# Kernel optimization log

Measured on AMD Instinct MI355X. Metric: run time of the kernel, lower is better.

Reference implementation:

```python
import jax, jax.numpy as jnp
import numpy as np

HIDDEN = 2048
NUM_HEADS = 32
NUM_KV_HEADS = 8
HEAD_DIM = 64
HEADS_PER_KV = NUM_HEADS // NUM_KV_HEADS


def setup_inputs() -> dict:
    key = jax.random.key(0)
    ks = jax.random.split(key, 5)
    B, S = 2, 2048
    sd = 1.0 / np.sqrt(HIDDEN)
    x = jax.random.normal(ks[0], (B, S, HIDDEN), dtype=jnp.float32)
    wq = jax.random.normal(ks[1], (HIDDEN, NUM_HEADS * HEAD_DIM), dtype=jnp.float32) * sd
    wk = jax.random.normal(ks[2], (HIDDEN, NUM_KV_HEADS * HEAD_DIM), dtype=jnp.float32) * sd
    wv = jax.random.normal(ks[3], (HIDDEN, NUM_KV_HEADS * HEAD_DIM), dtype=jnp.float32) * sd
    wo = jax.random.normal(ks[4], (NUM_HEADS * HEAD_DIM, HIDDEN), dtype=jnp.float32) * sd
    return {"x": x, "wq": wq, "wk": wk, "wv": wv, "wo": wo}


def reference(x, wq, wk, wv, wo):
    B, S, _ = x.shape
    scale = 1.0 / np.sqrt(HEAD_DIM)
    # projections; self-attention (is_cross=False) so kv source = x
    q = (x @ wq).reshape(B, S, NUM_HEADS, HEAD_DIM)          # [B,S,H,D]
    k = (x @ wk).reshape(B, S, NUM_KV_HEADS, HEAD_DIM)        # [B,S,Hkv,D]
    v = (x @ wv).reshape(B, S, NUM_KV_HEADS, HEAD_DIM)
    # GQA: group query heads per kv head instead of repeating K/V
    q = q.reshape(B, S, NUM_KV_HEADS, HEADS_PER_KV, HEAD_DIM)
    # scores: [B, Hkv, G, Sq, Skv]
    scores = jnp.einsum('bqhgd,bkhd->bhgqk', q, k) * scale
    probs = jax.nn.softmax(scores, axis=-1)
    out = jnp.einsum('bhgqk,bkhd->bqhgd', probs, v)
    out = out.reshape(B, S, NUM_HEADS * HEAD_DIM)
    return out @ wo
```

## Files before the change

kernel.cpp:

```cpp
#include <hip/hip_runtime.h>
#include <hip/hip_bf16.h>


#define S_LEN 2048

typedef __hip_bfloat16 bf16;
using bf16x8 = __attribute__((ext_vector_type(8))) __bf16;
using f32x4  = __attribute__((ext_vector_type(4))) float;

__device__ inline unsigned short bf16_bits(float f) {
    union { __hip_bfloat16 h; unsigned short u; } cv;
    cv.h = __float2bfloat16(f);
    return cv.u;
}

__device__ inline float bits_to_f(unsigned short u) {
    union { __hip_bfloat16 h; unsigned short u; } cv;
    cv.u = u;
    return __bfloat162float(cv.h);
}

__device__ inline unsigned int cvt_pk_bf16(float lo, float hi) {
    unsigned int r;
    asm volatile("v_cvt_pk_bf16_f32 %0, %1, %2" : "=v"(r) : "v"(lo), "v"(hi));
    return r;
}

__device__ inline bf16x8 load_cvt8(const float* __restrict__ p) {
    f32x4 a = *(const f32x4*)p;
    f32x4 b = *(const f32x4*)(p + 4);
    union { bf16x8 v; unsigned short u[8]; } r;
    r.u[0] = bf16_bits(a[0]); r.u[1] = bf16_bits(a[1]);
    r.u[2] = bf16_bits(a[2]); r.u[3] = bf16_bits(a[3]);
    r.u[4] = bf16_bits(b[0]); r.u[5] = bf16_bits(b[1]);
    r.u[6] = bf16_bits(b[2]); r.u[7] = bf16_bits(b[3]);
    return r.v;
}

__device__ inline void gload_lds16(const bf16* g, bf16* l) {
    __builtin_amdgcn_global_load_lds((const __attribute__((address_space(1))) void*)g,
                                     (__attribute__((address_space(3))) void*)l,
                                     16, 0, 0);
}

__global__ __launch_bounds__(256) void prep_k(const float* __restrict__ x,
                                              const float* __restrict__ wq,
                                              const float* __restrict__ wk,
                                              const float* __restrict__ wv,
                                              bf16* __restrict__ xb,
                                              bf16* __restrict__ wqT,
                                              bf16* __restrict__ wkT,
                                              bf16* __restrict__ wvT) {
    __shared__ float tile[32][33];
    int bid = blockIdx.x;
    if (bid < 4096) {
        int i = bid * 256 + threadIdx.x;
        *(bf16x8*)(xb + (size_t)i * 8) = load_cvt8(x + (size_t)i * 8);
        return;
    }
    const float* in; bf16* out; int R, C, local;
    if (bid < 8192)      { local = bid - 4096; in = wq; out = wqT; R = 2048; C = 2048; }
    else if (bid < 9216) { local = bid - 8192; in = wk; out = wkT; R = 2048; C = 512;  }
    else                 { local = bid - 9216; in = wv; out = wvT; R = 2048; C = 512;  }
    int gx = C >> 5;
    int c0 = (local % gx) * 32, r0 = (local / gx) * 32;
    int tx = threadIdx.x & 31, ty = threadIdx.x >> 5;
#pragma unroll
    for (int p = 0; p < 4; ++p)
        tile[ty + p * 8][tx] = in[(size_t)(r0 + ty + p * 8) * C + c0 + tx];
    __syncthreads();
#pragma unroll
    for (int p = 0; p < 4; ++p)
        out[(size_t)(c0 + ty + p * 8) * R + r0 + tx] = __float2bfloat16(tile[tx][ty + p * 8]);
}

__global__ __launch_bounds__(256) void transpose_k(const float* __restrict__ in,
                                                   bf16* __restrict__ out,
                                                   int R, int C) {
    __shared__ float tile[32][33];
    int tx = threadIdx.x & 31, ty = threadIdx.x >> 5;
    int r0 = blockIdx.y * 32, c0 = blockIdx.x * 32;
#pragma unroll
    for (int p = 0; p < 4; ++p)
        tile[ty + p * 8][tx] = in[(size_t)(r0 + ty + p * 8) * C + c0 + tx];
    __syncthreads();
#pragma unroll
    for (int p = 0; p < 4; ++p)
        out[(size_t)(c0 + ty + p * 8) * R + r0 + tx] = __float2bfloat16(tile[tx][ty + p * 8]);
}

__global__ __launch_bounds__(256) void gemm_k(const bf16* __restrict__ A,
                                              const bf16* __restrict__ Bt,
                                              void* __restrict__ Cv,
                                              void* __restrict__ Cv2,
                                              void* __restrict__ Cv3,
                                              int M, int N, int K, int mode) {
    __shared__ bf16 As[128 * 32];
    __shared__ bf16 Bs[128 * 32];
    int tid  = threadIdx.x;
    int lane = tid & 63, wave = tid >> 6;
    int quad = lane >> 4, r = lane & 15;
    int wm = (wave >> 1) * 64, wn = (wave & 1) * 64;

    int nwg  = gridDim.x * gridDim.y;
    int flat = blockIdx.y * gridDim.x + blockIdx.x;
    int cpx  = nwg >> 3;
    int swz  = (flat & 7) * cpx + (flat >> 3);
    int m0 = (swz / gridDim.x) * 128, n0 = (swz % gridDim.x) * 128;

    f32x4 acc[4][4];
#pragma unroll
    for (int i = 0; i < 4; ++i)
#pragma unroll
        for (int j = 0; j < 4; ++j) acc[i][j] = (f32x4)0.0f;

    int rg = lane >> 2;
    int ck = (lane & 3) << 3;

    for (int k0 = 0; k0 < K; k0 += 32) {
#pragma unroll
        for (int g = 0; g < 2; ++g) {
            int grp = wave * 2 + g;
            int row = grp * 16 + rg;
            gload_lds16(A  + (size_t)(m0 + row) * K + k0 + ck, &As[grp * 512]);
            gload_lds16(Bt + (size_t)(n0 + row) * K + k0 + ck, &Bs[grp * 512]);
        }
        __syncthreads();
        bf16x8 af[4], bfr[4];
#pragma unroll
        for (int mt = 0; mt < 4; ++mt) af[mt]  = *(const bf16x8*)&As[(wm + mt * 16 + r) * 32 + quad * 8];
#pragma unroll
        for (int nt = 0; nt < 4; ++nt) bfr[nt] = *(const bf16x8*)&Bs[(wn + nt * 16 + r) * 32 + quad * 8];
#pragma unroll
        for (int mt = 0; mt < 4; ++mt)
#pragma unroll
            for (int nt = 0; nt < 4; ++nt)
                acc[mt][nt] = __builtin_amdgcn_mfma_f32_16x16x32_bf16(af[mt], bfr[nt], acc[mt][nt], 0, 0, 0);
        __syncthreads();
    }

    if (mode == 2) {
        float* C = (float*)Cv;
#pragma unroll
        for (int mt = 0; mt < 4; ++mt)
#pragma unroll
            for (int nt = 0; nt < 4; ++nt) {
                int row = m0 + wm + mt * 16 + quad * 4;
                int col = n0 + wn + nt * 16 + r;
#pragma unroll
                for (int i = 0; i < 4; ++i)
                    C[(size_t)(row + i) * N + col] = acc[mt][nt][i];
            }
    } else {
        if (n0 < 2048) {
            bf16* C = (bf16*)Cv;
#pragma unroll
            for (int mt = 0; mt < 4; ++mt)
#pragma unroll
                for (int nt = 0; nt < 4; ++nt) {
                    int row = m0 + wm + mt * 16 + quad * 4;
                    int col = n0 + wn + nt * 16 + r;
#pragma unroll
                    for (int i = 0; i < 4; ++i)
                        C[(size_t)(row + i) * 2048 + col] = __float2bfloat16(acc[mt][nt][i]);
                }
        } else if (n0 < 2560) {
            bf16* C = (bf16*)Cv2;
#pragma unroll
            for (int mt = 0; mt < 4; ++mt)
#pragma unroll
                for (int nt = 0; nt < 4; ++nt) {
                    int row = m0 + wm + mt * 16 + quad * 4;
                    int col = n0 - 2048 + wn + nt * 16 + r;
#pragma unroll
                    for (int i = 0; i < 4; ++i)
                        C[(size_t)(row + i) * 512 + col] = __float2bfloat16(acc[mt][nt][i]);
                }
        } else {
            unsigned short* C = (unsigned short*)Cv3;
#pragma unroll
            for (int mt = 0; mt < 4; ++mt)
#pragma unroll
                for (int nt = 0; nt < 4; ++nt) {
                    int rowb = m0 + wm + mt * 16 + quad * 4;
                    int col  = n0 - 2560 + wn + nt * 16 + r;
                    int b = rowb >> 11, s = rowb & 2047;
                    ushort4 pk;
                    pk.x = bf16_bits(acc[mt][nt][0]);
                    pk.y = bf16_bits(acc[mt][nt][1]);
                    pk.z = bf16_bits(acc[mt][nt][2]);
                    pk.w = bf16_bits(acc[mt][nt][3]);
                    *(ushort4*)(C + (size_t)(b * 512 + col) * 2048 + s) = pk;
                }
        }
    }
}

__global__ __launch_bounds__(256, 2) void attn_k(const bf16* __restrict__ Qin,
                                                 const bf16* __restrict__ Kb,
                                                 const bf16* __restrict__ Vt,
                                                 bf16* __restrict__ Aout) {
    __shared__ bf16 Ks[4][64 * 64];
    __shared__ bf16 Vs[4][64 * 64];
    __shared__ bf16 Pl[4][16 * 64];

    int tid = threadIdx.x, lane = tid & 63, w = tid >> 6;
    int quad = lane >> 4, r = lane & 15;
    int qt = blockIdx.x, h = blockIdx.y, b = blockIdx.z;
    int hk = h >> 2;

    bf16x8 qf[4][2];
#pragma unroll
    for (int s = 0; s < 4; ++s) {
        int q0 = qt * 256 + s * 64 + w * 16;
#pragma unroll
        for (int f = 0; f < 2; ++f) {
            bf16x8 v = *(const bf16x8*)(Qin + (size_t)(b * S_LEN + q0 + r) * 2048 + h * 64 + f * 32 + quad * 8);
            union { bf16x8 v; unsigned short u[8]; } i_, o_;
            i_.v = v;
#pragma unroll
            for (int j = 0; j < 8; ++j) o_.u[j] = bf16_bits(bits_to_f(i_.u[j]) * 0.125f);
            qf[s][f] = o_.v;
        }
    }

    bf16x8 onesf;
    {
        union { bf16x8 v; unsigned short u[8]; } o_;
#pragma unroll
        for (int j = 0; j < 8; ++j) o_.u[j] = 0x3F80;
        onesf = o_.v;
    }

    const bf16* Kbase = Kb + (size_t)b * S_LEN * 512 + hk * 64;
    const bf16* Vbase = Vt + (size_t)(b * 512 + hk * 64) * 2048;
    char* myP = (char*)&Pl[w][0];

    int srow   = lane >> 3;
    int schunk = (lane & 7) ^ srow;
    int wrow0 = w * 16, wrow1 = w * 16 + 8;

    f32x4 oacc[4][4];
#pragma unroll
    for (int s = 0; s < 4; ++s)
#pragma unroll
        for (int dt = 0; dt < 4; ++dt) oacc[s][dt] = (f32x4)0.0f;
    f32x4 lacc[4];
#pragma unroll
    for (int s = 0; s < 4; ++s) lacc[s] = (f32x4)0.0f;

#define STAGE(SB, K0)                                                                    \
    do {                                                                                 \
        gload_lds16(Kbase + (size_t)((K0) + wrow0 + srow) * 512 + schunk * 8,            \
                    &Ks[SB][wrow0 * 64]);                                                \
        gload_lds16(Kbase + (size_t)((K0) + wrow1 + srow) * 512 + schunk * 8,            \
                    &Ks[SB][wrow1 * 64]);                                                \
        gload_lds16(Vbase + (size_t)(wrow0 + srow) * 2048 + (K0) + schunk * 8,           \
                    &Vs[SB][wrow0 * 64]);                                                \
        gload_lds16(Vbase + (size_t)(wrow1 + srow) * 2048 + (K0) + schunk * 8,           \
                    &Vs[SB][wrow1 * 64]);                                                \
    } while (0)

    STAGE(0, 0);
    STAGE(1, 64);
    __syncthreads();

#define SUB_STEP(SB)                                                                     \
    do {                                                                                 \
        f32x4 S[4][4];                                                                   \
        {                                                                                \
            bf16x8 kf[4][2];                                                             \
            _Pragma("unroll")                                                            \
            for (int t = 0; t < 4; ++t)                                                  \
                _Pragma("unroll")                                                        \
                for (int half = 0; half < 2; ++half)                                     \
                    kf[t][half] = *(const bf16x8*)&Ks[SB][(t * 16 + r) * 64 +            \
                                                    ((half * 4 + quad) ^ (r & 7)) * 8];  \
            __builtin_amdgcn_s_setprio(1);                                               \
            _Pragma("unroll")                                                            \
            for (int s = 0; s < 4; ++s)                                                  \
                _Pragma("unroll")                                                        \
                for (int t = 0; t < 4; ++t) {                                            \
                    f32x4 z = (f32x4)0.0f;                                               \
                    z = __builtin_amdgcn_mfma_f32_16x16x32_bf16(kf[t][0], qf[s][0], z, 0, 0, 0); \
                    z = __builtin_amdgcn_mfma_f32_16x16x32_bf16(kf[t][1], qf[s][1], z, 0, 0, 0); \
                    S[s][t] = z;                                                         \
                }                                                                        \
            __builtin_amdgcn_s_setprio(0);                                               \
        }                                                                                \
        bf16x8 vf[4][2];                                                                 \
        _Pragma("unroll")                                                                \
        for (int dt = 0; dt < 4; ++dt)                                                   \
            _Pragma("unroll")                                                            \
            for (int half = 0; half < 2; ++half)                                         \
                vf[dt][half] = *(const bf16x8*)&Vs[SB][(dt * 16 + r) * 64 +              \
                                                ((half * 4 + quad) ^ (r & 7)) * 8];      \
        _Pragma("unroll")                                                                \
        for (int s = 0; s < 4; ++s) {                                                    \
            float p[16];                                                                 \
            _Pragma("unroll")                                                            \
            for (int t = 0; t < 4; ++t)                                                  \
                _Pragma("unroll")                                                        \
                for (int i = 0; i < 4; ++i) p[t * 4 + i] = __expf(S[s][t][i]);           \
            _Pragma("unroll")                                                            \
            for (int t = 0; t < 4; ++t) {                                                \
                uint2 pk;                                                                \
                pk.x = cvt_pk_bf16(p[t * 4 + 0], p[t * 4 + 1]);                          \
                pk.y = cvt_pk_bf16(p[t * 4 + 2], p[t * 4 + 3]);                          \
                *(uint2*)(myP + r * 128 + (((t * 2 + (quad >> 1)) ^ (r & 7)) * 16) +     \
                          (quad & 1) * 8) = pk;                                          \
            }                                                                            \
            bf16x8 pf0 = *(const bf16x8*)(myP + r * 128 + ((quad ^ (r & 7)) * 16));      \
            bf16x8 pf1 = *(const bf16x8*)(myP + r * 128 + (((4 + quad) ^ (r & 7)) * 16));\
            __builtin_amdgcn_s_setprio(1);                                               \
            lacc[s] = __builtin_amdgcn_mfma_f32_16x16x32_bf16(pf0, onesf, lacc[s], 0, 0, 0); \
            lacc[s] = __builtin_amdgcn_mfma_f32_16x16x32_bf16(pf1, onesf, lacc[s], 0, 0, 0); \
            _Pragma("unroll")                                                            \
            for (int dt = 0; dt < 4; ++dt) {                                             \
                f32x4 o = oacc[s][dt];                                                   \
                o = __builtin_amdgcn_mfma_f32_16x16x32_bf16(pf0, vf[dt][0], o, 0, 0, 0); \
                o = __builtin_amdgcn_mfma_f32_16x16x32_bf16(pf1, vf[dt][1], o, 0, 0, 0); \
                oacc[s][dt] = o;                                                         \
            }                                                                            \
            __builtin_amdgcn_s_setprio(0);                                               \
        }                                                                                \
    } while (0)

#define ATTN_TILE(B0, B1, PB0, PB1, K0)                                                  \
    do {                                                                                 \
        int k0n_ = (K0) + 128;                                                           \
        if (k0n_ < S_LEN) {                                                              \
            STAGE(PB0, k0n_);                                                            \
            STAGE(PB1, k0n_ + 64);                                                       \
        }                                                                                \
        SUB_STEP(B0);                                                                    \
        SUB_STEP(B1);                                                                    \
        __syncthreads();                                                                 \
    } while (0)

    for (int itp = 0; itp < S_LEN / 256; ++itp) {
        int base = itp * 256;
        ATTN_TILE(0, 1, 2, 3, base);
        ATTN_TILE(2, 3, 0, 1, base + 128);
    }
#undef ATTN_TILE
#undef SUB_STEP
#undef STAGE

#pragma unroll
    for (int s = 0; s < 4; ++s) {
        int q0 = qt * 256 + s * 64 + w * 16;
        float linv[4];
#pragma unroll
        for (int i = 0; i < 4; ++i) linv[i] = 1.0f / lacc[s][i];
#pragma unroll
        for (int dt = 0; dt < 4; ++dt)
#pragma unroll
            for (int i = 0; i < 4; ++i)
                Aout[(size_t)(b * S_LEN + q0 + quad * 4 + i) * 2048 + h * 64 + dt * 16 + r] =
                    __float2bfloat16(oacc[s][dt][i] * linv[i]);
    }
}

extern "C" void kernel_launch(void* const* d_in, const int* in_sizes, int n_in,
                              void* d_out, int out_size, void* d_ws, size_t ws_size,
                              hipStream_t stream) {
    const float* x  = (const float*)d_in[0];
    const float* wq = (const float*)d_in[1];
    const float* wk = (const float*)d_in[2];
    const float* wv = (const float*)d_in[3];
    const float* wo = (const float*)d_in[4];
    char* ws = (char*)d_ws;

    bf16* wqT  = (bf16*)(ws + 0);
    bf16* wkT  = (bf16*)(ws + 8388608);
    bf16* wvT  = (bf16*)(ws + 10485760);
    bf16* attn = (bf16*)(ws + 0);
    bf16* Kb   = (bf16*)(ws + 16777216);
    bf16* Vtb  = (bf16*)(ws + 20971520);
    bf16* woT  = (bf16*)(ws + 16777216);
    bf16* Qb   = (bf16*)d_out;
    bf16* xb   = (bf16*)((char*)d_out + 16777216);

    prep_k<<<dim3(10240), 256, 0, stream>>>(x, wq, wk, wv, xb, wqT, wkT, wvT);

    gemm_k<<<dim3(24, 32), 256, 0, stream>>>(xb, wqT, Qb, Kb, Vtb, 4096, 3072, 2048, 3);

    attn_k<<<dim3(8, 32, 2), 256, 0, stream>>>(Qb, Kb, Vtb, attn);

    transpose_k<<<dim3(64, 64), 256, 0, stream>>>(wo, woT, 2048, 2048);

    gemm_k<<<dim3(16, 32), 256, 0, stream>>>(attn, woT, d_out, nullptr, nullptr, 4096, 2048, 2048, 2);
}
```

Before: 333.1 us.

## Pipeline K/V staging per 64-key sub-tile with partial vmcnt waits

Restructures the attention inner loop from 128-key tiles with a full __syncthreads (which waits for all outstanding global loads) into per-64-key steps that prefetch two sub-tiles ahead. Each step waits only until at most 4 loads remain outstanding (s_waitcnt vmcnt(4)) before a raw barrier, so the next buffer's loads stay in flight. The loop is peeled so the tail drains with vmcnt(0). This aims to overlap global-to-LDS loads with MFMA work, but it relies on exact vmcnt accounting and adds more frequent barriers.

```diff
diff --git a/kernel.cpp b/kernel.cpp
--- a/kernel.cpp
+++ b/kernel.cpp
@@ -261,9 +261,22 @@
                     &Vs[SB][wrow1 * 64]);                                                \
     } while (0)
 
+#define SYNC_VM4()                                                                       \
+    do {                                                                                 \
+        asm volatile("s_waitcnt vmcnt(4)" ::: "memory");                                 \
+        __builtin_amdgcn_s_barrier();                                                    \
+        __builtin_amdgcn_sched_barrier(0);                                               \
+    } while (0)
+#define SYNC_VM0()                                                                       \
+    do {                                                                                 \
+        asm volatile("s_waitcnt vmcnt(0)" ::: "memory");                                 \
+        __builtin_amdgcn_s_barrier();                                                    \
+        __builtin_amdgcn_sched_barrier(0);                                               \
+    } while (0)
+
     STAGE(0, 0);
     STAGE(1, 64);
-    __syncthreads();
+    SYNC_VM4();
 
 #define SUB_STEP(SB)                                                                     \
     do {                                                                                 \
@@ -326,26 +339,30 @@
         }                                                                                \
     } while (0)
 
-#define ATTN_TILE(B0, B1, PB0, PB1, K0)                                                  \
+#define ATTN_STEP4(BUF, PBUF, K0)                                                        \
     do {                                                                                 \
-        int k0n_ = (K0) + 128;                                                           \
-        if (k0n_ < S_LEN) {                                                              \
-            STAGE(PB0, k0n_);                                                            \
-            STAGE(PB1, k0n_ + 64);                                                       \
-        }                                                                                \
-        SUB_STEP(B0);                                                                    \
-        SUB_STEP(B1);                                                                    \
-        __syncthreads();                                                                 \
+        STAGE(PBUF, (K0) + 128);                                                         \
+        SUB_STEP(BUF);                                                                   \
+        SYNC_VM4();                                                                      \
     } while (0)
 
-    for (int itp = 0; itp < S_LEN / 256; ++itp) {
-        int base = itp * 256;
-        ATTN_TILE(0, 1, 2, 3, base);
-        ATTN_TILE(2, 3, 0, 1, base + 128);
-    }
-#undef ATTN_TILE
+    for (int i = 0; i < 7; ++i) {
+        int base = i * 256;
+        ATTN_STEP4(0, 2, base + 0);
+        ATTN_STEP4(1, 3, base + 64);
+        ATTN_STEP4(2, 0, base + 128);
+        ATTN_STEP4(3, 1, base + 192);
+    }
+    ATTN_STEP4(0, 2, 1792);
+    ATTN_STEP4(1, 3, 1856);
+    SUB_STEP(2);
+    SYNC_VM0();
+    SUB_STEP(3);
+#undef ATTN_STEP4
 #undef SUB_STEP
 #undef STAGE
+#undef SYNC_VM4
+#undef SYNC_VM0
 
 #pragma unroll
     for (int s = 0; s < 4; ++s) {
```

New measurement: 368.4 us. +10.6%, slower.
